# Optimization experiments

Measured on AMD Instinct MI355X. Metric: run time of the kernel, lower is better.

## Reference

```python
import jax, jax.numpy as jnp
import numpy as np

PAD_IDX = 0
VOCAB = 60
HIDDEN = 128
BATCH = 1024
SEQ = 256


def setup_inputs() -> dict:
    key = jax.random.key(0)
    ks = jax.random.split(key, 6)
    x = jax.random.randint(ks[0], (BATCH, SEQ), 0, VOCAB, dtype=jnp.int64 if jax.config.jax_enable_x64 else jnp.int32)
    lengths = jax.random.randint(ks[1], (BATCH,), 1, SEQ + 1, dtype=x.dtype)
    emb = jax.random.normal(ks[2], (VOCAB, HIDDEN), dtype=jnp.float32) * 0.1
    emb = emb.at[PAD_IDX].set(0.0)  # nn.Embedding padding_idx row is zero
    W_ih = jax.random.normal(ks[3], (HIDDEN, HIDDEN), dtype=jnp.float32) * (1.0 / np.sqrt(HIDDEN))
    W_hh = jax.random.normal(ks[4], (HIDDEN, HIDDEN), dtype=jnp.float32) * (1.0 / np.sqrt(HIDDEN))
    W_fc = jax.random.normal(ks[5], (VOCAB, HIDDEN), dtype=jnp.float32) * (1.0 / np.sqrt(HIDDEN))
    b_fc = jnp.zeros((VOCAB,), dtype=jnp.float32)
    return {"x": x, "lengths": lengths, "emb": emb, "W_ih": W_ih,
            "W_hh": W_hh, "W_fc": W_fc, "b_fc": b_fc}


def reference(x, lengths, emb, W_ih, W_hh, W_fc, b_fc):
    embedded = emb[x]                      # [B, T, H]
    B = embedded.shape[0]
    h0 = jnp.zeros((B, HIDDEN), dtype=embedded.dtype)

    def step(h_prev, x_t):
        # z_t = x_t @ W_ih^T + h_prev @ W_hh^T ; h_t = tanh(z_t)
        h_t = jnp.tanh(x_t @ W_ih.T + h_prev @ W_hh.T)
        return h_t, h_t

    _, hs = jax.lax.scan(step, h0, jnp.swapaxes(embedded, 0, 1))  # hs: [T, B, H]
    outputs = jnp.swapaxes(hs, 0, 1)       # [B, T, H]
    last_out = jnp.take_along_axis(outputs, (lengths - 1)[:, None, None], axis=1)[:, 0, :]  # [B, H]
    return last_out @ W_fc.T + b_fc[None, :]
```

## Files before the change

### kernel.cpp

```cpp
#include <hip/hip_runtime.h>
#include <hip/hip_bf16.h>

#define BATCH 1024
#define SEQ 256
#define HIDDEN 128
#define VOCAB 60
#define ROWS 4
#define CHUNK 16
#define ASTRIDE 144
#define RSTR 136

typedef _Float16 f16x8 __attribute__((ext_vector_type(8)));
typedef _Float16 f16x4 __attribute__((ext_vector_type(4)));
typedef float f32x4 __attribute__((ext_vector_type(4)));

__device__ __forceinline__ float fast_tanh(float x) {
    float e = __builtin_amdgcn_exp2f(x * 2.8853900817779268f);
    return __builtin_fmaf(-2.0f, __builtin_amdgcn_rcpf(e + 1.0f), 1.0f);
}

__global__ void rnn_prep_embw(const float* __restrict__ emb,
                              const float* __restrict__ W_ih,
                              float* __restrict__ embW) {
    const int v = blockIdx.x;
    const int i = threadIdx.x;
    __shared__ __align__(16) float e[HIDDEN];
    e[i] = emb[v * HIDDEN + i];
    __syncthreads();
    const float4* wrow = (const float4*)(W_ih + i * HIDDEN);
    const float4* e4 = (const float4*)e;
    float a0 = 0.f, a1 = 0.f, a2 = 0.f, a3 = 0.f;
#pragma unroll
    for (int j = 0; j < HIDDEN / 4; ++j) {
        float4 w = wrow[j];
        float4 h = e4[j];
        a0 += w.x * h.x; a1 += w.y * h.y; a2 += w.z * h.z; a3 += w.w * h.w;
    }
    embW[v * HIDDEN + i] = (a0 + a1) + (a2 + a3);
}

__global__ void __launch_bounds__(512)
rnn_mfma(const int* __restrict__ x, const int* __restrict__ lengths,
         const float* __restrict__ embW, const float* __restrict__ W_hh,
         const float* __restrict__ W_fc, const float* __restrict__ b_fc,
         float* __restrict__ out) {
    const int tid = threadIdx.x;
    const int wave = tid >> 6;
    const int lane = tid & 63;
    const int q = lane >> 4;
    const int r16 = lane & 15;
    const int r4 = r16 & 3;
    const int c0 = wave * 16;
    const int b0 = blockIdx.x * ROWS;

    __shared__ __align__(16) float ring[CHUNK][ROWS][RSTR];
    __shared__ __align__(16) _Float16 Ah[2][ROWS][ASTRIDE];
    __shared__ int xs[ROWS][SEQ + 1];
    __shared__ __align__(16) float hfin[ROWS][HIDDEN];
    __shared__ int lenbuf[ROWS];

    for (int idx = tid; idx < ROWS * SEQ; idx += 512) {
        int r = idx >> 8, t = idx & (SEQ - 1);
        xs[r][t] = x[(b0 + r) * SEQ + t];
    }
    if (tid < ROWS) lenbuf[tid] = lengths[b0 + tid];
    for (int idx = tid; idx < (int)(sizeof(Ah) / 4); idx += 512)
        ((int*)Ah)[idx] = 0;

    f16x8 Wf[4];
    {
        const float* wrow = W_hh + (c0 + r16) * HIDDEN + q * 8;
#pragma unroll
        for (int kc = 0; kc < 4; ++kc) {
            const float* p = wrow + kc * 32;
#pragma unroll
            for (int j = 0; j < 8; ++j) Wf[kc][j] = (_Float16)p[j];
        }
    }

    __syncthreads();

    const int mylen = lenbuf[r4];
    int lenmax = 0;
#pragma unroll
    for (int r = 0; r < ROWS; ++r) lenmax = max(lenmax, lenbuf[r]);

    const int s_c4 = tid & 31;
    const int s_r = (tid >> 5) & 3;
    const int s_tp = tid >> 7;

    f32x4 rg[4];
#pragma unroll
    for (int k = 0; k < 4; ++k) {
        int tp = s_tp + 4 * k;
        int tok = xs[s_r][tp];
        rg[k] = *(const f32x4*)(embW + tok * HIDDEN + s_c4 * 4);
    }

    int cur = 0;
    f32x4 cap = {0.f, 0.f, 0.f, 0.f};

    for (int t0 = 0; t0 < lenmax; t0 += CHUNK) {
#pragma unroll
        for (int k = 0; k < 4; ++k)
            *(f32x4*)&ring[s_tp + 4 * k][s_r][s_c4 * 4] = rg[k];
        __syncthreads();

        if (t0 + CHUNK < lenmax) {
            const int t0n = t0 + CHUNK;
#pragma unroll
            for (int k = 0; k < 4; ++k) {
                int tp = s_tp + 4 * k;
                int tok = xs[s_r][t0n + tp];
                rg[k] = *(const f32x4*)(embW + tok * HIDDEN + s_c4 * 4);
            }
        }

        const int tend = (lenmax - t0 < CHUNK) ? lenmax - t0 : CHUNK;
        for (int tt = 0; tt < tend; ++tt) {
            const _Float16* hb = &Ah[cur][r4][q * 8];
            f16x8 H0 = *(const f16x8*)(hb + 0);
            f16x8 H1 = *(const f16x8*)(hb + 32);
            f16x8 H2 = *(const f16x8*)(hb + 64);
            f16x8 H3 = *(const f16x8*)(hb + 96);

            f32x4 a = *(const f32x4*)&ring[tt][r4][c0 + 4 * q];
            f32x4 d = {0.f, 0.f, 0.f, 0.f};
            a = __builtin_amdgcn_mfma_f32_16x16x32_f16(Wf[0], H0, a, 0, 0, 0);
            d = __builtin_amdgcn_mfma_f32_16x16x32_f16(Wf[2], H2, d, 0, 0, 0);
            a = __builtin_amdgcn_mfma_f32_16x16x32_f16(Wf[1], H1, a, 0, 0, 0);
            d = __builtin_amdgcn_mfma_f32_16x16x32_f16(Wf[3], H3, d, 0, 0, 0);
            f32x4 z = a + d;

            f32x4 th;
            th[0] = fast_tanh(z[0]);
            th[1] = fast_tanh(z[1]);
            th[2] = fast_tanh(z[2]);
            th[3] = fast_tanh(z[3]);

            uint2 pk;
            pk.x = __builtin_bit_cast(unsigned int, __builtin_amdgcn_cvt_pkrtz(th[0], th[1]));
            pk.y = __builtin_bit_cast(unsigned int, __builtin_amdgcn_cvt_pkrtz(th[2], th[3]));

            const int nxt = cur ^ 1;
            if (r16 < ROWS)
                *(uint2*)&Ah[nxt][r16][c0 + 4 * q] = pk;
            if (t0 + tt + 1 == mylen) cap = th;
            __syncthreads();
            cur = nxt;
        }
    }

    if (r16 < ROWS)
        *(f32x4*)&hfin[r16][c0 + 4 * q] = cap;
    __syncthreads();

    const int r = tid >> 7;
    const int c = tid & 127;
    if (c < VOCAB) {
        const float4* hv = (const float4*)hfin[r];
        const float4* wf = (const float4*)(W_fc + c * HIDDEN);
        float a0 = 0.f, a1 = 0.f, a2 = 0.f, a3 = 0.f;
#pragma unroll
        for (int j = 0; j < HIDDEN / 4; ++j) {
            float4 h = hv[j];
            float4 w = wf[j];
            a0 += h.x * w.x; a1 += h.y * w.y; a2 += h.z * w.z; a3 += h.w * w.w;
        }
        out[(b0 + r) * VOCAB + c] = (a0 + a1) + (a2 + a3) + b_fc[c];
    }
}

extern "C" void kernel_launch(void* const* d_in, const int* in_sizes, int n_in,
                              void* d_out, int out_size, void* d_ws, size_t ws_size,
                              hipStream_t stream) {
    const int* x = (const int*)d_in[0];
    const int* lengths = (const int*)d_in[1];
    const float* emb = (const float*)d_in[2];
    const float* W_ih = (const float*)d_in[3];
    const float* W_hh = (const float*)d_in[4];
    const float* W_fc = (const float*)d_in[5];
    const float* b_fc = (const float*)d_in[6];
    float* out = (float*)d_out;

    float* embW = (float*)d_ws;

    rnn_prep_embw<<<VOCAB, HIDDEN, 0, stream>>>(emb, W_ih, embW);
    rnn_mfma<<<BATCH / ROWS, 512, 0, stream>>>(x, lengths, embW, W_hh, W_fc, b_fc, out);
}
```

Measured before the change: 161.2 us.

## Halve rows per block and give each wave two MFMA column tiles

The batch is now split into blocks of 2 rows with 256 threads instead of 4 rows with 512 threads. Each wave now computes two 16-column output tiles per step, which doubles the MFMA count per wave and exposes independent MFMA chains. The per-step barrier spans 4 waves instead of 8, and each block's serial length is the max over 2 sequences rather than 4. The cost is more weight registers per lane and twice as many blocks sharing each CU.

```diff
diff --git a/kernel.cpp b/kernel.cpp
--- a/kernel.cpp
+++ b/kernel.cpp
@@ -5,13 +5,12 @@
 #define SEQ 256
 #define HIDDEN 128
 #define VOCAB 60
-#define ROWS 4
+#define ROWS 2
 #define CHUNK 16
-#define ASTRIDE 144
-#define RSTR 136
+#define ASTRIDE 160
+#define RSTR 144
 
 typedef _Float16 f16x8 __attribute__((ext_vector_type(8)));
-typedef _Float16 f16x4 __attribute__((ext_vector_type(4)));
 typedef float f32x4 __attribute__((ext_vector_type(4)));
 
 __device__ __forceinline__ float fast_tanh(float x) {
@@ -39,7 +38,7 @@
     embW[v * HIDDEN + i] = (a0 + a1) + (a2 + a3);
 }
 
-__global__ void __launch_bounds__(512)
+__global__ void __launch_bounds__(256)
 rnn_mfma(const int* __restrict__ x, const int* __restrict__ lengths,
          const float* __restrict__ embW, const float* __restrict__ W_hh,
          const float* __restrict__ W_fc, const float* __restrict__ b_fc,
@@ -49,56 +48,54 @@
     const int lane = tid & 63;
     const int q = lane >> 4;
     const int r16 = lane & 15;
-    const int r4 = r16 & 3;
-    const int c0 = wave * 16;
+    const int r2 = r16 & 1;
+    const int c0 = wave * 32;
     const int b0 = blockIdx.x * ROWS;
 
     __shared__ __align__(16) float ring[CHUNK][ROWS][RSTR];
     __shared__ __align__(16) _Float16 Ah[2][ROWS][ASTRIDE];
-    __shared__ int xs[ROWS][SEQ + 1];
+    __shared__ int xs[ROWS][SEQ + 8];
     __shared__ __align__(16) float hfin[ROWS][HIDDEN];
     __shared__ int lenbuf[ROWS];
 
-    for (int idx = tid; idx < ROWS * SEQ; idx += 512) {
+    for (int idx = tid; idx < ROWS * SEQ; idx += 256) {
         int r = idx >> 8, t = idx & (SEQ - 1);
         xs[r][t] = x[(b0 + r) * SEQ + t];
     }
     if (tid < ROWS) lenbuf[tid] = lengths[b0 + tid];
-    for (int idx = tid; idx < (int)(sizeof(Ah) / 4); idx += 512)
+    for (int idx = tid; idx < (int)(sizeof(Ah) / 4); idx += 256)
         ((int*)Ah)[idx] = 0;
 
-    f16x8 Wf[4];
-    {
-        const float* wrow = W_hh + (c0 + r16) * HIDDEN + q * 8;
+    f16x8 Wf[2][4];
+#pragma unroll
+    for (int nt = 0; nt < 2; ++nt) {
+        const float* wrow = W_hh + (c0 + 16 * nt + r16) * HIDDEN + q * 8;
 #pragma unroll
         for (int kc = 0; kc < 4; ++kc) {
             const float* p = wrow + kc * 32;
 #pragma unroll
-            for (int j = 0; j < 8; ++j) Wf[kc][j] = (_Float16)p[j];
+            for (int j = 0; j < 8; ++j) Wf[nt][kc][j] = (_Float16)p[j];
         }
     }
 
     __syncthreads();
 
-    const int mylen = lenbuf[r4];
-    int lenmax = 0;
-#pragma unroll
-    for (int r = 0; r < ROWS; ++r) lenmax = max(lenmax, lenbuf[r]);
+    const int mylen = lenbuf[r2];
+    const int lenmax = max(lenbuf[0], lenbuf[1]);
 
     const int s_c4 = tid & 31;
-    const int s_r = (tid >> 5) & 3;
-    const int s_tp = tid >> 7;
+    const int s_r = (tid >> 5) & 1;
+    const int s_tp = tid >> 6;
 
     f32x4 rg[4];
 #pragma unroll
     for (int k = 0; k < 4; ++k) {
-        int tp = s_tp + 4 * k;
-        int tok = xs[s_r][tp];
+        int tok = xs[s_r][s_tp + 4 * k];
         rg[k] = *(const f32x4*)(embW + tok * HIDDEN + s_c4 * 4);
     }
 
     int cur = 0;
-    f32x4 cap = {0.f, 0.f, 0.f, 0.f};
+    f32x4 cap0 = {0.f, 0.f, 0.f, 0.f}, cap1 = {0.f, 0.f, 0.f, 0.f};
 
     for (int t0 = 0; t0 < lenmax; t0 += CHUNK) {
 #pragma unroll
@@ -110,49 +107,61 @@
             const int t0n = t0 + CHUNK;
 #pragma unroll
             for (int k = 0; k < 4; ++k) {
-                int tp = s_tp + 4 * k;
-                int tok = xs[s_r][t0n + tp];
+                int tok = xs[s_r][t0n + s_tp + 4 * k];
                 rg[k] = *(const f32x4*)(embW + tok * HIDDEN + s_c4 * 4);
             }
         }
 
         const int tend = (lenmax - t0 < CHUNK) ? lenmax - t0 : CHUNK;
         for (int tt = 0; tt < tend; ++tt) {
-            const _Float16* hb = &Ah[cur][r4][q * 8];
+            const _Float16* hb = &Ah[cur][r2][q * 8];
             f16x8 H0 = *(const f16x8*)(hb + 0);
             f16x8 H1 = *(const f16x8*)(hb + 32);
             f16x8 H2 = *(const f16x8*)(hb + 64);
             f16x8 H3 = *(const f16x8*)(hb + 96);
 
-            f32x4 a = *(const f32x4*)&ring[tt][r4][c0 + 4 * q];
-            f32x4 d = {0.f, 0.f, 0.f, 0.f};
-            a = __builtin_amdgcn_mfma_f32_16x16x32_f16(Wf[0], H0, a, 0, 0, 0);
-            d = __builtin_amdgcn_mfma_f32_16x16x32_f16(Wf[2], H2, d, 0, 0, 0);
-            a = __builtin_amdgcn_mfma_f32_16x16x32_f16(Wf[1], H1, a, 0, 0, 0);
-            d = __builtin_amdgcn_mfma_f32_16x16x32_f16(Wf[3], H3, d, 0, 0, 0);
-            f32x4 z = a + d;
+            f32x4 a0 = *(const f32x4*)&ring[tt][r2][c0 + 4 * q];
+            f32x4 a1 = *(const f32x4*)&ring[tt][r2][c0 + 16 + 4 * q];
+            f32x4 d0 = {0.f, 0.f, 0.f, 0.f}, d1 = {0.f, 0.f, 0.f, 0.f};
+            a0 = __builtin_amdgcn_mfma_f32_16x16x32_f16(Wf[0][0], H0, a0, 0, 0, 0);
+            a1 = __builtin_amdgcn_mfma_f32_16x16x32_f16(Wf[1][0], H0, a1, 0, 0, 0);
+            d0 = __builtin_amdgcn_mfma_f32_16x16x32_f16(Wf[0][2], H2, d0, 0, 0, 0);
+            d1 = __builtin_amdgcn_mfma_f32_16x16x32_f16(Wf[1][2], H2, d1, 0, 0, 0);
+            a0 = __builtin_amdgcn_mfma_f32_16x16x32_f16(Wf[0][1], H1, a0, 0, 0, 0);
+            a1 = __builtin_amdgcn_mfma_f32_16x16x32_f16(Wf[1][1], H1, a1, 0, 0, 0);
+            d0 = __builtin_amdgcn_mfma_f32_16x16x32_f16(Wf[0][3], H3, d0, 0, 0, 0);
+            d1 = __builtin_amdgcn_mfma_f32_16x16x32_f16(Wf[1][3], H3, d1, 0, 0, 0);
+            f32x4 z0 = a0 + d0;
+            f32x4 z1 = a1 + d1;
 
-            f32x4 th;
-            th[0] = fast_tanh(z[0]);
-            th[1] = fast_tanh(z[1]);
-            th[2] = fast_tanh(z[2]);
-            th[3] = fast_tanh(z[3]);
+            f32x4 th0, th1;
+#pragma unroll
+            for (int v = 0; v < 4; ++v) {
+                th0[v] = fast_tanh(z0[v]);
+                th1[v] = fast_tanh(z1[v]);
+            }
 
-            uint2 pk;
-            pk.x = __builtin_bit_cast(unsigned int, __builtin_amdgcn_cvt_pkrtz(th[0], th[1]));
-            pk.y = __builtin_bit_cast(unsigned int, __builtin_amdgcn_cvt_pkrtz(th[2], th[3]));
+            uint2 p0, p1;
+            p0.x = __builtin_bit_cast(unsigned int, __builtin_amdgcn_cvt_pkrtz(th0[0], th0[1]));
+            p0.y = __builtin_bit_cast(unsigned int, __builtin_amdgcn_cvt_pkrtz(th0[2], th0[3]));
+            p1.x = __builtin_bit_cast(unsigned int, __builtin_amdgcn_cvt_pkrtz(th1[0], th1[1]));
+            p1.y = __builtin_bit_cast(unsigned int, __builtin_amdgcn_cvt_pkrtz(th1[2], th1[3]));
 
             const int nxt = cur ^ 1;
-            if (r16 < ROWS)
-                *(uint2*)&Ah[nxt][r16][c0 + 4 * q] = pk;
-            if (t0 + tt + 1 == mylen) cap = th;
+            if (r16 < ROWS) {
+                *(uint2*)&Ah[nxt][r16][c0 + 4 * q] = p0;
+                *(uint2*)&Ah[nxt][r16][c0 + 16 + 4 * q] = p1;
+            }
+            if (t0 + tt + 1 == mylen) { cap0 = th0; cap1 = th1; }
             __syncthreads();
             cur = nxt;
         }
     }
 
-    if (r16 < ROWS)
-        *(f32x4*)&hfin[r16][c0 + 4 * q] = cap;
+    if (r16 < ROWS) {
+        *(f32x4*)&hfin[r16][c0 + 4 * q] = cap0;
+        *(f32x4*)&hfin[r16][c0 + 16 + 4 * q] = cap1;
+    }
     __syncthreads();
 
     const int r = tid >> 7;
@@ -186,5 +195,5 @@
     float* embW = (float*)d_ws;
 
     rnn_prep_embw<<<VOCAB, HIDDEN, 0, stream>>>(emb, W_ih, embW);
-    rnn_mfma<<<BATCH / ROWS, 512, 0, stream>>>(x, lengths, embW, W_hh, W_fc, b_fc, out);
+    rnn_mfma<<<BATCH / ROWS, 256, 0, stream>>>(x, lengths, embW, W_hh, W_fc, b_fc, out);
 }
```

Result: slower. 197.4 us (+22.5%).
